# Kernel optimization log

Hardware: AMD Instinct MI355X
Metric: run time of the kernel (lower is better)

Reference implementation:

```python
import jax, jax.numpy as jnp
import numpy as np

LAMBDA_1 = 1.0
LAMBDA_2 = 0.5


def setup_inputs() -> dict:
    key = jax.random.key(0)
    k1, k2, k3, k4, k5 = jax.random.split(key, 5)
    N_TRAIN, N_UNL, C = 4096, 32768, 1000
    G, K = 512, 64
    return {
        "train_logits": jax.random.normal(k1, (N_TRAIN, C), dtype=jnp.float32),
        "train_targets": jax.random.randint(k2, (N_TRAIN,), 0, C, dtype=jnp.int64),
        "unlabeled_logits": jax.random.normal(k3, (N_UNL, C), dtype=jnp.float32),
        "centroid_ids": jax.random.randint(k4, (G,), 0, N_TRAIN, dtype=jnp.int64),
        "member_ids": jax.random.randint(k5, (G, K), 0, N_UNL, dtype=jnp.int64),
    }


def reference(train_logits, train_targets, unlabeled_logits, centroid_ids, member_ids):
    N_unl = unlabeled_logits.shape[0]
    G, K = member_ids.shape

    # --- cross-entropy (mean) ---
    logp = jax.nn.log_softmax(train_logits, axis=-1)
    ce = -jnp.mean(jnp.take_along_axis(logp, train_targets[:, None], axis=1))

    # --- gather group tensors ---
    centroids = train_logits[centroid_ids]          # [G, C]
    members = unlabeled_logits[member_ids]          # [G, K, C]

    # --- alignment: sum_g sum_k ||centroid_g - member_gk||_2 / N_unl ---
    align = jnp.sum(jnp.linalg.norm(centroids[:, None, :] - members, axis=-1)) / N_unl

    # --- robustness: per-group upper-triangle pairwise L2 sums / (K * N_unl) ---
    sq = jnp.sum(members * members, axis=-1)                       # [G, K]
    gram = jnp.einsum("gkc,glc->gkl", members, members)            # [G, K, K]
    d2 = jnp.maximum(sq[:, :, None] + sq[:, None, :] - 2.0 * gram, 0.0)
    dist = jnp.sqrt(jnp.where(d2 > 0, d2, 1.0)) * (d2 > 0)         # safe sqrt
    iu = jnp.triu(jnp.ones((K, K), dtype=dist.dtype), k=1)         # i < j pairs
    robust = jnp.sum(dist * iu) / (K * N_unl)

    return ce + LAMBDA_1 * align + LAMBDA_2 * robust
```

## Files before the change

### kernel.cpp

```cpp
#include <hip/hip_runtime.h>

#define N_TRAIN 4096
#define N_UNL   32768
#define C_DIM   1000
#define G_GRP   512
#define K_MEM   64

#define CE_BLOCKS (N_TRAIN / 16)
#define NBLK      (G_GRP + CE_BLOCKS)

#define CHUNKS  8
#define CCOLS   128
#define PITCH_B 272
#define ROWS    80

typedef short        short8 __attribute__((ext_vector_type(8)));
typedef float        f32x4  __attribute__((ext_vector_type(4)));
typedef unsigned int u32x2  __attribute__((ext_vector_type(2)));
typedef unsigned int u32x4  __attribute__((ext_vector_type(4)));

__device__ __forceinline__ unsigned int pack_bf(float a, float b) {
    unsigned int ua = __float_as_uint(a) + 0x8000u;
    unsigned int ub = __float_as_uint(b) + 0x8000u;
    return (ua >> 16) | (ub & 0xffff0000u);
}

__global__ __launch_bounds__(256) void fused_kernel(const float* __restrict__ train,
                                                    const int*   __restrict__ targets,
                                                    const float* __restrict__ unl,
                                                    const int*   __restrict__ cids,
                                                    const int*   __restrict__ mids,
                                                    float* __restrict__ out) {
    __shared__ __align__(16) unsigned short bf[ROWS * (PITCH_B / 2)];
    __shared__ int   ids_sh[K_MEM];
    __shared__ float sq_sh[K_MEM];
    __shared__ float red_sh[256];
    __shared__ float sqc_sh;

    const int tid  = threadIdx.x;
    const int w    = tid >> 6;
    const int lane = tid & 63;

    if (blockIdx.x >= G_GRP) {
        const int blk = (int)blockIdx.x - G_GRP;
        float ce = 0.f;
        for (int r4 = 0; r4 < 4; ++r4) {
            const int row = blk * 16 + w * 4 + r4;
            const float* rp = train + (long)row * C_DIM;
            float x[16];
#pragma unroll
            for (int i = 0; i < 16; ++i) {
                int c = lane + i * 64;
                x[i] = (c < C_DIM) ? rp[c] : -1e30f;
            }
            float m = x[0];
#pragma unroll
            for (int i = 1; i < 16; ++i) m = fmaxf(m, x[i]);
#pragma unroll
            for (int off = 32; off > 0; off >>= 1) m = fmaxf(m, __shfl_xor(m, off, 64));
            float s = 0.f;
#pragma unroll
            for (int i = 0; i < 16; ++i) s += __expf(x[i] - m);
#pragma unroll
            for (int off = 32; off > 0; off >>= 1) s += __shfl_xor(s, off, 64);
            if (lane == 0) {
                int t = targets[row];
                ce += -(rp[t] - m - __logf(s));
            }
        }
        if (lane == 0) red_sh[w] = ce;
        __syncthreads();
        if (tid == 0)
            atomicAdd(out, (red_sh[0] + red_sh[1] + red_sh[2] + red_sh[3]) *
                           (1.0f / (float)N_TRAIN));
        return;
    }

    const int g    = blockIdx.x;
    const int quad = lane >> 4;
    const int c16  = lane & 15;

    if (tid < 255)
        *(u32x4*)((char*)bf + 65 * PITCH_B + tid * 16) = (u32x4){0, 0, 0, 0};
    if (tid < K_MEM) ids_sh[tid] = mids[g * K_MEM + tid];
    __syncthreads();

    const int rgrp = tid >> 5;
    const int l32  = tid & 31;
    const int cid  = cids[g];

    const float* srcb[8];
#pragma unroll
    for (int i = 0; i < 8; ++i)
        srcb[i] = unl + (long)ids_sh[rgrp + 8 * i] * C_DIM + l32 * 4;
    const float* csrc = train + (long)cid * C_DIM + l32 * 4;

    f32x4 acc[4], accC, accD;
#pragma unroll
    for (int t = 0; t < 4; ++t) acc[t] = (f32x4){0.f, 0.f, 0.f, 0.f};
    accC = (f32x4){0.f, 0.f, 0.f, 0.f};
    accD = (f32x4){0.f, 0.f, 0.f, 0.f};

    const float4 z4 = make_float4(0.f, 0.f, 0.f, 0.f);

    float4 mreg[8];
    float4 creg;

    {
        const bool v = (l32 * 4 < C_DIM);
#pragma unroll
        for (int i = 0; i < 8; ++i) mreg[i] = v ? *(const float4*)(srcb[i]) : z4;
        if (tid < 32) creg = *(const float4*)(csrc);
    }

    for (int ch = 0; ch < CHUNKS; ++ch) {
        __syncthreads();

#pragma unroll
        for (int i = 0; i < 8; ++i) {
            u32x2 h = {pack_bf(mreg[i].x, mreg[i].y), pack_bf(mreg[i].z, mreg[i].w)};
            *(u32x2*)((char*)bf + (rgrp + 8 * i) * PITCH_B + l32 * 8) = h;
        }
        if (tid < 32) {
            u32x2 h = {pack_bf(creg.x, creg.y), pack_bf(creg.z, creg.w)};
            *(u32x2*)((char*)bf + 64 * PITCH_B + tid * 8) = h;
        }
        __syncthreads();

        if (ch + 1 < CHUNKS) {
            const int col = (ch + 1) * CCOLS + l32 * 4;
            const bool v = (col < C_DIM);
            const long off = (long)(ch + 1) * CCOLS;
#pragma unroll
            for (int i = 0; i < 8; ++i) mreg[i] = v ? *(const float4*)(srcb[i] + off) : z4;
            if (tid < 32) creg = v ? *(const float4*)(csrc + off) : z4;
        }

#pragma unroll
        for (int s = 0; s < 4; ++s) {
            const int kbb = s * 64 + quad * 16;
            const char* base = (const char*)bf;
            short8 b0 = *(const short8*)(base + (0 * 16 + c16) * PITCH_B + kbb);
            short8 b1 = *(const short8*)(base + (1 * 16 + c16) * PITCH_B + kbb);
            short8 b2 = *(const short8*)(base + (2 * 16 + c16) * PITCH_B + kbb);
            short8 b3 = *(const short8*)(base + (3 * 16 + c16) * PITCH_B + kbb);
            short8 aM = *(const short8*)(base + (w * 16 + c16) * PITCH_B + kbb);
            short8 aC = *(const short8*)(base + (64 + c16) * PITCH_B + kbb);
            acc[0] = __builtin_amdgcn_mfma_f32_16x16x32_bf16(aM, b0, acc[0], 0, 0, 0);
            acc[1] = __builtin_amdgcn_mfma_f32_16x16x32_bf16(aM, b1, acc[1], 0, 0, 0);
            acc[2] = __builtin_amdgcn_mfma_f32_16x16x32_bf16(aM, b2, acc[2], 0, 0, 0);
            acc[3] = __builtin_amdgcn_mfma_f32_16x16x32_bf16(aM, b3, acc[3], 0, 0, 0);
            accC   = __builtin_amdgcn_mfma_f32_16x16x32_bf16(aC, aM, accC, 0, 0, 0);
            if (w == 0)
                accD = __builtin_amdgcn_mfma_f32_16x16x32_bf16(aC, aC, accD, 0, 0, 0);
        }
    }

#pragma unroll
    for (int t = 0; t < 4; ++t) {
        if (t == w) {
#pragma unroll
            for (int r = 0; r < 4; ++r)
                if (c16 == quad * 4 + r) sq_sh[w * 16 + c16] = acc[t][r];
        }
    }
    if (tid == 0) sqc_sh = accD[0];
    __syncthreads();

    float local = 0.f;
    if (quad == 0) {
        const int j = w * 16 + c16;
        const float d2 = sqc_sh + sq_sh[j] - 2.f * accC[0];
        if (d2 > 0.f) local += sqrtf(d2) * (1.0f / (float)N_UNL);
    }
#pragma unroll
    for (int t = 0; t < 4; ++t) {
#pragma unroll
        for (int r = 0; r < 4; ++r) {
            const int i = w * 16 + quad * 4 + r;
            const int j = t * 16 + c16;
            if (j > i) {
                const float d2 = sq_sh[i] + sq_sh[j] - 2.f * acc[t][r];
                if (d2 > 0.f)
                    local += sqrtf(d2) * (0.5f / ((float)K_MEM * (float)N_UNL));
            }
        }
    }

    red_sh[tid] = local;
    __syncthreads();
#pragma unroll
    for (int s = 128; s > 0; s >>= 1) {
        if (tid < s) red_sh[tid] += red_sh[tid + s];
        __syncthreads();
    }
    if (tid == 0) atomicAdd(out, red_sh[0]);
}

extern "C" void kernel_launch(void* const* d_in, const int* in_sizes, int n_in,
                              void* d_out, int out_size, void* d_ws, size_t ws_size,
                              hipStream_t stream) {
    (void)in_sizes; (void)n_in; (void)d_ws; (void)ws_size;
    const float* train_logits  = (const float*)d_in[0];
    const int*   train_targets = (const int*)d_in[1];
    const float* unl           = (const float*)d_in[2];
    const int*   centroid_ids  = (const int*)d_in[3];
    const int*   member_ids    = (const int*)d_in[4];
    float* out = (float*)d_out;

    hipMemsetAsync(out, 0, (size_t)out_size * sizeof(float), stream);
    fused_kernel<<<NBLK, 256, 0, stream>>>(train_logits, train_targets, unl,
                                           centroid_ids, member_ids, out);
}
```

Before: 210.4 us.

## Double-buffer LDS tiles and prefetch two chunks ahead in group loop

The bf16 staging buffer in shared memory becomes two alternating buffers, and global loads for member and centroid rows are issued two chunks ahead in two register sets. This removes one block-wide barrier per chunk and gives global loads more time in flight. The cost is more registers for the extra prefetch set and double the LDS footprint, which may reduce occupancy. The zero-fill of the padding rows is dropped; those rows only affect output rows that are never read.

```diff
diff --git a/kernel.cpp b/kernel.cpp
--- a/kernel.cpp
+++ b/kernel.cpp
@@ -17,7 +17,6 @@
 typedef short        short8 __attribute__((ext_vector_type(8)));
 typedef float        f32x4  __attribute__((ext_vector_type(4)));
 typedef unsigned int u32x2  __attribute__((ext_vector_type(2)));
-typedef unsigned int u32x4  __attribute__((ext_vector_type(4)));
 
 __device__ __forceinline__ unsigned int pack_bf(float a, float b) {
     unsigned int ua = __float_as_uint(a) + 0x8000u;
@@ -31,7 +30,7 @@
                                                     const int*   __restrict__ cids,
                                                     const int*   __restrict__ mids,
                                                     float* __restrict__ out) {
-    __shared__ __align__(16) unsigned short bf[ROWS * (PITCH_B / 2)];
+    __shared__ __align__(16) unsigned short bf[2][ROWS * (PITCH_B / 2)];
     __shared__ int   ids_sh[K_MEM];
     __shared__ float sq_sh[K_MEM];
     __shared__ float red_sh[256];
@@ -80,8 +79,6 @@
     const int quad = lane >> 4;
     const int c16  = lane & 15;
 
-    if (tid < 255)
-        *(u32x4*)((char*)bf + 65 * PITCH_B + tid * 16) = (u32x4){0, 0, 0, 0};
     if (tid < K_MEM) ids_sh[tid] = mids[g * K_MEM + tid];
     __syncthreads();
 
@@ -103,43 +100,46 @@
 
     const float4 z4 = make_float4(0.f, 0.f, 0.f, 0.f);
 
-    float4 mreg[8];
-    float4 creg;
-
-    {
-        const bool v = (l32 * 4 < C_DIM);
-#pragma unroll
-        for (int i = 0; i < 8; ++i) mreg[i] = v ? *(const float4*)(srcb[i]) : z4;
-        if (tid < 32) creg = *(const float4*)(csrc);
+    float4 mreg[2][8];
+    float4 creg[2];
+
+#pragma unroll
+    for (int p = 0; p < 2; ++p) {
+        const long off = (long)p * CCOLS;
+#pragma unroll
+        for (int i = 0; i < 8; ++i) mreg[p][i] = *(const float4*)(srcb[i] + off);
+        if (tid < 32) creg[p] = *(const float4*)(csrc + off);
     }
 
     for (int ch = 0; ch < CHUNKS; ++ch) {
+        const int buf = ch & 1;
+#pragma unroll
+        for (int i = 0; i < 8; ++i) {
+            u32x2 h = {pack_bf(mreg[buf][i].x, mreg[buf][i].y),
+                       pack_bf(mreg[buf][i].z, mreg[buf][i].w)};
+            *(u32x2*)((char*)bf[buf] + (rgrp + 8 * i) * PITCH_B + l32 * 8) = h;
+        }
+        if (tid < 32) {
+            u32x2 h = {pack_bf(creg[buf].x, creg[buf].y),
+                       pack_bf(creg[buf].z, creg[buf].w)};
+            *(u32x2*)((char*)bf[buf] + 64 * PITCH_B + tid * 8) = h;
+        }
         __syncthreads();
 
-#pragma unroll
-        for (int i = 0; i < 8; ++i) {
-            u32x2 h = {pack_bf(mreg[i].x, mreg[i].y), pack_bf(mreg[i].z, mreg[i].w)};
-            *(u32x2*)((char*)bf + (rgrp + 8 * i) * PITCH_B + l32 * 8) = h;
-        }
-        if (tid < 32) {
-            u32x2 h = {pack_bf(creg.x, creg.y), pack_bf(creg.z, creg.w)};
-            *(u32x2*)((char*)bf + 64 * PITCH_B + tid * 8) = h;
-        }
-        __syncthreads();
-
-        if (ch + 1 < CHUNKS) {
-            const int col = (ch + 1) * CCOLS + l32 * 4;
+        if (ch + 2 < CHUNKS) {
+            const int col = (ch + 2) * CCOLS + l32 * 4;
             const bool v = (col < C_DIM);
-            const long off = (long)(ch + 1) * CCOLS;
-#pragma unroll
-            for (int i = 0; i < 8; ++i) mreg[i] = v ? *(const float4*)(srcb[i] + off) : z4;
-            if (tid < 32) creg = v ? *(const float4*)(csrc + off) : z4;
+            const long off = (long)(ch + 2) * CCOLS;
+#pragma unroll
+            for (int i = 0; i < 8; ++i)
+                mreg[buf][i] = v ? *(const float4*)(srcb[i] + off) : z4;
+            if (tid < 32) creg[buf] = v ? *(const float4*)(csrc + off) : z4;
         }
 
 #pragma unroll
         for (int s = 0; s < 4; ++s) {
             const int kbb = s * 64 + quad * 16;
-            const char* base = (const char*)bf;
+            const char* base = (const char*)bf[buf];
             short8 b0 = *(const short8*)(base + (0 * 16 + c16) * PITCH_B + kbb);
             short8 b1 = *(const short8*)(base + (1 * 16 + c16) * PITCH_B + kbb);
             short8 b2 = *(const short8*)(base + (2 * 16 + c16) * PITCH_B + kbb);
```

After: 212.1 us. No clear change (+0.8%).
